# Kernel optimization log

Hardware: AMD Instinct MI355X
Metric: run time of the kernel (lower is better)

## Reference

```python
import jax, jax.numpy as jnp
from jax import lax
import numpy as np

W = 64  # window_size

def setup_inputs() -> dict:
    key = jax.random.key(0)
    x = jax.random.normal(key, (262144, 32), dtype=jnp.float32)
    return {"x": x}

def _roll(x, init, op):
    # sliding window of size W along axis 0, stride 1, VALID -> (T-W+1, F)
    return lax.reduce_window(x, init, op, window_dimensions=(W, 1),
                             window_strides=(1, 1), padding="VALID")

def reference(x):
    # drop_na=True, stride=1, keep_original=False,
    # statistics = [mean, std, min, max, sum] concatenated on last axis.
    s = _roll(x, jnp.float32(0), lax.add)          # rolling sum
    s2 = _roll(x * x, jnp.float32(0), lax.add)     # rolling sum of squares
    mean = s / W
    # tf.math.reduce_std is population std: sqrt(E[x^2] - E[x]^2)
    std = jnp.sqrt(jnp.maximum(s2 / W - mean * mean, 0.0))
    mn = _roll(x, jnp.float32(jnp.inf), lax.min)
    mx = _roll(x, jnp.float32(-jnp.inf), lax.max)
    return jnp.concatenate([mean, std, mn, mx, s], axis=-1)
```

## Files before the change

kernel.cpp:

```cpp
#include <hip/hip_runtime.h>
#include <math.h>


#define WINW 64
#define RCH 8
#define NF 32
#define CHUNKS_PER_BLK 8
#define ROWS_PER_BLK (CHUNKS_PER_BLK * RCH)
#define STAGE_ROWS (ROWS_PER_BLK + WINW)

__global__ __launch_bounds__(256, 8) void rolling_stats_kernel(
    const float* __restrict__ x, float* __restrict__ out, int N, int T_out) {
  __shared__ float tile[STAGE_ROWS * NF];

  int t0_blk = blockIdx.x * ROWS_PER_BLK;

  const float4* xv = (const float4*)x;
  float4* tv = (float4*)tile;
#pragma unroll
  for (int it = 0; it < (STAGE_ROWS * NF / 4) / 256; ++it) {
    int f = it * 256 + (int)threadIdx.x;
    int r = f >> 3;
    int gr = t0_blk + r;
    gr = gr < N ? gr : N - 1;
    tv[f] = xv[(size_t)gr * (NF / 4) + (f & 7)];
  }
  __syncthreads();

  int c = (int)threadIdx.x & (NF - 1);
  int lr0 = ((int)threadIdx.x >> 5) * RCH;
  int t0 = t0_blk + lr0;
  const float* tc = tile + c;

  float smin[RCH], smax[RCH];
  float ssum = 0.f, ssq = 0.f;
  float rmin = INFINITY, rmax = -INFINITY;

#pragma unroll
  for (int j = WINW - 1; j >= RCH; --j) {
    float a = tc[(lr0 + j) * NF];
    rmin = fminf(rmin, a);
    rmax = fmaxf(rmax, a);
    ssum += a;
    ssq = fmaf(a, a, ssq);
  }
#pragma unroll
  for (int j = RCH - 1; j >= 0; --j) {
    float a = tc[(lr0 + j) * NF];
    rmin = fminf(rmin, a);
    rmax = fmaxf(rmax, a);
    ssum += a;
    ssq = fmaf(a, a, ssq);
    smin[j] = rmin;
    smax[j] = rmax;
  }

  float pmin = INFINITY, pmax = -INFINITY;
  float wsum = ssum, wsq = ssq;
  float* o = out + (size_t)t0 * (5 * NF) + c;
#pragma unroll
  for (int j = 0; j < RCH; ++j) {
    if (j > 0) {
      float bnew = tc[(lr0 + WINW - 1 + j) * NF];
      float aold = tc[(lr0 + j - 1) * NF];
      pmin = fminf(pmin, bnew);
      pmax = fmaxf(pmax, bnew);
      wsum += bnew - aold;
      wsq = fmaf(bnew, bnew, wsq);
      wsq = fmaf(-aold, aold, wsq);
    }
    if (t0 + j < T_out) {
      float wmin = fminf(smin[j], pmin);
      float wmax = fmaxf(smax[j], pmax);
      float mean = wsum * 0.015625f;
      float var = fmaf(-mean, mean, wsq * 0.015625f);
      var = fmaxf(var, 0.f);
      float sd = sqrtf(var);
      float* orow = o + (size_t)j * (5 * NF);
      orow[0 * NF] = mean;
      orow[1 * NF] = sd;
      orow[2 * NF] = wmin;
      orow[3 * NF] = wmax;
      orow[4 * NF] = wsum;
    }
  }
}

extern "C" void kernel_launch(void* const* d_in, const int* in_sizes, int n_in,
                              void* d_out, int out_size, void* d_ws,
                              size_t ws_size, hipStream_t stream) {
  const float* x = (const float*)d_in[0];
  float* out = (float*)d_out;
  int N = in_sizes[0] / NF;
  int T_out = N - (WINW - 1);
  int nblocks = (T_out + ROWS_PER_BLK - 1) / ROWS_PER_BLK;
  rolling_stats_kernel<<<nblocks, 256, 0, stream>>>(x, out, N, T_out);
}
```

Baseline: 184.6 us.

## Vectorize per-thread rolling stats to 4 features with 256-row blocks and nontemporal stores

Each thread now handles 4 adjacent features through float4 vectors instead of one scalar feature. The block covers 256 output rows instead of 64, so the 63-row halo is reloaded less often relative to useful work. Outputs are written as 128-bit nontemporal stores, and launch bounds drop to 3 blocks per CU. The trade-off is higher register use (vector smin/smax arrays), more LDS per block, and lower occupancy.

Measured after the change: 193.6 us. 4.9% more time.

```diff
diff --git a/kernel.cpp b/kernel.cpp
--- a/kernel.cpp
+++ b/kernel.cpp
@@ -2,86 +2,110 @@
 #include <math.h>
 
 
+typedef float vf4 __attribute__((ext_vector_type(4)));
+
 #define WINW 64
 #define RCH 8
 #define NF 32
-#define CHUNKS_PER_BLK 8
-#define ROWS_PER_BLK (CHUNKS_PER_BLK * RCH)
+#define ROWS_PER_BLK 256
 #define STAGE_ROWS (ROWS_PER_BLK + WINW)
 
-__global__ __launch_bounds__(256, 8) void rolling_stats_kernel(
+__device__ __forceinline__ vf4 v4min(vf4 a, vf4 b) {
+  vf4 r;
+  r.x = fminf(a.x, b.x); r.y = fminf(a.y, b.y);
+  r.z = fminf(a.z, b.z); r.w = fminf(a.w, b.w);
+  return r;
+}
+__device__ __forceinline__ vf4 v4max(vf4 a, vf4 b) {
+  vf4 r;
+  r.x = fmaxf(a.x, b.x); r.y = fmaxf(a.y, b.y);
+  r.z = fmaxf(a.z, b.z); r.w = fmaxf(a.w, b.w);
+  return r;
+}
+__device__ __forceinline__ vf4 v4fma(vf4 a, vf4 b, vf4 c) {
+  vf4 r;
+  r.x = fmaf(a.x, b.x, c.x); r.y = fmaf(a.y, b.y, c.y);
+  r.z = fmaf(a.z, b.z, c.z); r.w = fmaf(a.w, b.w, c.w);
+  return r;
+}
+__device__ __forceinline__ vf4 v4sqrt(vf4 a) {
+  vf4 r;
+  r.x = sqrtf(a.x); r.y = sqrtf(a.y);
+  r.z = sqrtf(a.z); r.w = sqrtf(a.w);
+  return r;
+}
+
+__global__ __launch_bounds__(256, 3) void rolling_stats_kernel(
     const float* __restrict__ x, float* __restrict__ out, int N, int T_out) {
-  __shared__ float tile[STAGE_ROWS * NF];
+  __shared__ vf4 tile[STAGE_ROWS * 8];
 
   int t0_blk = blockIdx.x * ROWS_PER_BLK;
 
-  const float4* xv = (const float4*)x;
-  float4* tv = (float4*)tile;
+  const vf4* xv = (const vf4*)x;
 #pragma unroll
-  for (int it = 0; it < (STAGE_ROWS * NF / 4) / 256; ++it) {
+  for (int it = 0; it < (STAGE_ROWS * 8) / 256; ++it) {
     int f = it * 256 + (int)threadIdx.x;
     int r = f >> 3;
+    int q = f & 7;
     int gr = t0_blk + r;
     gr = gr < N ? gr : N - 1;
-    tv[f] = xv[(size_t)gr * (NF / 4) + (f & 7)];
+    tile[f] = xv[(size_t)gr * 8 + q];
   }
   __syncthreads();
 
-  int c = (int)threadIdx.x & (NF - 1);
-  int lr0 = ((int)threadIdx.x >> 5) * RCH;
+  int g = (int)threadIdx.x & 7;
+  int lr0 = ((int)threadIdx.x >> 3) * RCH;
   int t0 = t0_blk + lr0;
-  const float* tc = tile + c;
+  const vf4* tc = tile + g;
 
-  float smin[RCH], smax[RCH];
-  float ssum = 0.f, ssq = 0.f;
-  float rmin = INFINITY, rmax = -INFINITY;
+  vf4 smin[RCH], smax[RCH];
+  vf4 ssum = {0.f, 0.f, 0.f, 0.f};
+  vf4 ssq = {0.f, 0.f, 0.f, 0.f};
+  vf4 rmin = {INFINITY, INFINITY, INFINITY, INFINITY};
+  vf4 rmax = {-INFINITY, -INFINITY, -INFINITY, -INFINITY};
 
 #pragma unroll
-  for (int j = WINW - 1; j >= RCH; --j) {
-    float a = tc[(lr0 + j) * NF];
-    rmin = fminf(rmin, a);
-    rmax = fmaxf(rmax, a);
+  for (int j = WINW - 1; j >= 0; --j) {
+    vf4 a = tc[(lr0 + j) * 8];
+    rmin = v4min(rmin, a);
+    rmax = v4max(rmax, a);
     ssum += a;
-    ssq = fmaf(a, a, ssq);
-  }
-#pragma unroll
-  for (int j = RCH - 1; j >= 0; --j) {
-    float a = tc[(lr0 + j) * NF];
-    rmin = fminf(rmin, a);
-    rmax = fmaxf(rmax, a);
-    ssum += a;
-    ssq = fmaf(a, a, ssq);
-    smin[j] = rmin;
-    smax[j] = rmax;
+    ssq = v4fma(a, a, ssq);
+    if (j < RCH) {
+      smin[j] = rmin;
+      smax[j] = rmax;
+    }
   }
 
-  float pmin = INFINITY, pmax = -INFINITY;
-  float wsum = ssum, wsq = ssq;
-  float* o = out + (size_t)t0 * (5 * NF) + c;
+  vf4 pmin = {INFINITY, INFINITY, INFINITY, INFINITY};
+  vf4 pmax = {-INFINITY, -INFINITY, -INFINITY, -INFINITY};
+  vf4 wsum = ssum, wsq = ssq;
+  float* ob = out + (size_t)t0 * (5 * NF) + 4 * g;
 #pragma unroll
   for (int j = 0; j < RCH; ++j) {
     if (j > 0) {
-      float bnew = tc[(lr0 + WINW - 1 + j) * NF];
-      float aold = tc[(lr0 + j - 1) * NF];
-      pmin = fminf(pmin, bnew);
-      pmax = fmaxf(pmax, bnew);
-      wsum += bnew - aold;
-      wsq = fmaf(bnew, bnew, wsq);
-      wsq = fmaf(-aold, aold, wsq);
+      vf4 b = tc[(lr0 + WINW - 1 + j) * 8];
+      vf4 a = tc[(lr0 + j - 1) * 8];
+      pmin = v4min(pmin, b);
+      pmax = v4max(pmax, b);
+      wsum += b - a;
+      wsq = v4fma(b, b, wsq);
+      wsq = v4fma(-a, a, wsq);
     }
     if (t0 + j < T_out) {
-      float wmin = fminf(smin[j], pmin);
-      float wmax = fmaxf(smax[j], pmax);
-      float mean = wsum * 0.015625f;
-      float var = fmaf(-mean, mean, wsq * 0.015625f);
-      var = fmaxf(var, 0.f);
-      float sd = sqrtf(var);
-      float* orow = o + (size_t)j * (5 * NF);
-      orow[0 * NF] = mean;
-      orow[1 * NF] = sd;
-      orow[2 * NF] = wmin;
-      orow[3 * NF] = wmax;
-      orow[4 * NF] = wsum;
+      vf4 wmin = v4min(smin[j], pmin);
+      vf4 wmax = v4max(smax[j], pmax);
+      vf4 mean = wsum * 0.015625f;
+      vf4 var = v4fma(-mean, mean, wsq * 0.015625f);
+      vf4 zero = {0.f, 0.f, 0.f, 0.f};
+      var = v4max(var, zero);
+      vf4 sd = v4sqrt(var);
+      float* orow = ob + (size_t)j * (5 * NF);
+      __builtin_nontemporal_store(mean, (vf4*)(orow + 0 * NF));
+      __builtin_nontemporal_store(sd,   (vf4*)(orow + 1 * NF));
+      __builtin_nontemporal_store(wmin, (vf4*)(orow + 2 * NF));
+      __builtin_nontemporal_store(wmax, (vf4*)(orow + 3 * NF));
+      __builtin_nontemporal_store(wsum, (vf4*)(orow + 4 * NF));
     }
   }
 }
```
